# Kernel optimization log

Measured on AMD Instinct MI355X. Metric: run time of the kernel, lower is better.

The kernel has to match this reference:

```python
import jax, jax.numpy as jnp
import numpy as np

SEQ_LEN = 2048
NUM_FILTERS = 24
INPUT_DIM = 256
OUTPUT_DIM = 256
BATCH = 2
N_FFT = 4096  # nearest power of two >= 2*SEQ_LEN - 1


def _spectral_filters(L, k):
    # Hankel matrix Z_{ij} = 2 / ((i+j)^3 - (i+j)), top-k eigvecs scaled by sigma^{1/4}
    e = np.arange(1, L + 1, dtype=np.float64)
    ipj = e[:, None] + e[None, :]
    Z = 2.0 / (ipj ** 3 - ipj)
    sigma, vecs = np.linalg.eigh(Z)
    phi = vecs[:, -k:] * (sigma[-k:] ** 0.25)
    return jnp.asarray(phi, dtype=jnp.float32)


def setup_inputs() -> dict:
    key = jax.random.key(0)
    k1, k2, k3 = jax.random.split(key, 3)
    scale = (NUM_FILTERS * INPUT_DIM) ** (-0.5)
    return {
        "x": jax.random.normal(k1, (BATCH, SEQ_LEN, INPUT_DIM), jnp.float32),
        "phi": _spectral_filters(SEQ_LEN, NUM_FILTERS),  # [L, K]
        "M_phi_plus": jax.random.normal(k2, (NUM_FILTERS, INPUT_DIM, OUTPUT_DIM), jnp.float32) * scale,
        "M_phi_minus": jax.random.normal(k3, (NUM_FILTERS, INPUT_DIM, OUTPUT_DIM), jnp.float32) * scale,
    }


def _convolve(x, phi, n):
    # Faithful port of flash-stu convolve() with use_approx=False.
    B, L, I = x.shape
    K = phi.shape[1]
    # alternating sign (+1, -1, +1, ...) along the sequence
    sgn = jnp.where(jnp.arange(L) % 2 == 0, 1.0, -1.0).astype(x.dtype)[None, :, None, None]  # (1,L,1,1)
    v = jnp.fft.rfft(phi, n=n, axis=0)[None, :, :, None, None]  # (1, n//2+1, K, 1, 1)
    u = jnp.broadcast_to(x[:, :, None, :, None], (B, L, K, I, 1))  # (B,L,K,I,1)
    U = jnp.concatenate([u, u * sgn[..., None]], axis=-1)          # (B,L,K,I,2)
    U_f = jnp.fft.rfft(U, n=n, axis=1)                             # (B,n//2+1,K,I,2)
    U_conv = jnp.fft.irfft(v * U_f, n=n, axis=1)[:, :L]            # (B,L,K,I,2)
    U_plus = U_conv[..., 0]
    U_minus = U_conv[..., 1] * sgn                                 # (B,L,K,I)
    return U_plus, U_minus


def reference(x, phi, M_phi_plus, M_phi_minus):
    U_plus, U_minus = _convolve(x, phi, N_FFT)
    spectral_plus = jnp.einsum('blki,kio->blo', U_plus, M_phi_plus)
    spectral_minus = jnp.einsum('blki,kio->blo', U_minus, M_phi_minus)
    return spectral_plus + spectral_minus
```

## Files before the change

kernel.cpp:

```cpp
#include <hip/hip_runtime.h>
#include <hip/hip_bf16.h>

#define SL 2048
#define NK 24
#define NI 256
#define NO 256
#define NB 2
#define NC 48
#define TD 64

typedef __bf16 bf16x8 __attribute__((ext_vector_type(8)));
typedef float f32x4 __attribute__((ext_vector_type(4)));
typedef unsigned short u16x8 __attribute__((ext_vector_type(8)));
typedef unsigned short ushort_t;
typedef unsigned int u32;

#define OFF_T   0ull
#define SZ_T    (35ull*48*64*64*2)
#define OFF_MT  (OFF_T + SZ_T)
#define SZ_MT   (48ull*256*256*2)
#define OFF_XB  (OFF_MT + SZ_MT)
#define SZ_XB   (2ull*2048*256*2)
#define OFF_YT  (OFF_XB + SZ_XB)
#define SZ_YT   (2ull*48*256*2048*2)
#define WS_NEED (OFF_YT + SZ_YT)

__device__ __forceinline__ unsigned short f2bf(float f) {
    unsigned int u = __float_as_uint(f);
    unsigned int r = (u + 0x7FFFu + ((u >> 16) & 1u)) >> 16;
    return (unsigned short)r;
}

__device__ __forceinline__ void glds16(ushort_t* l, const ushort_t* g) {
    __builtin_amdgcn_global_load_lds((const __attribute__((address_space(1))) u32*)g,
                                     (__attribute__((address_space(3))) u32*)l, 16, 0, 0);
}

__global__ void k_cvt_x(const float* __restrict__ x, ushort_t* __restrict__ xb) {
    int i = blockIdx.x * blockDim.x + threadIdx.x;
    float4 v = reinterpret_cast<const float4*>(x)[i];
    ushort4 o;
    o.x = f2bf(v.x); o.y = f2bf(v.y); o.z = f2bf(v.z); o.w = f2bf(v.w);
    reinterpret_cast<ushort4*>(xb)[i] = o;
}

__global__ void k_mt(const float* __restrict__ Mp, const float* __restrict__ Mm,
                     ushort_t* __restrict__ mt) {
    __shared__ float tile[64][65];
    int c = blockIdx.x, it = blockIdx.y, ot = blockIdx.z;
    int k = c >> 1;
    const float* M = (c & 1) ? Mm : Mp;
    int tid = threadIdx.x;
    int col = tid & 63, rq = tid >> 6;
    for (int rr = 0; rr < 64; rr += 4) {
        int i = rr + rq;
        tile[i][col] = M[((k * NI) + (it * 64 + i)) * NO + ot * 64 + col];
    }
    __syncthreads();
    for (int rr = 0; rr < 64; rr += 4) {
        int o = rr + rq;
        mt[((c * NO) + (ot * 64 + o)) * NI + it * 64 + col] = f2bf(tile[col][o]);
    }
}

__global__ void k_toep(const float* __restrict__ phi, ushort_t* __restrict__ T) {
    int d = (int)blockIdx.x - 3, c = blockIdx.y;
    int ti = threadIdx.x;
    int k = c >> 1, odd = c & 1;
    for (int li = 0; li < TD; ++li) {
        int s = d * TD + li - ti;
        float v = 0.f;
        if (s >= 0 && s < SL) {
            v = phi[s * NK + k];
            if (odd && (s & 1)) v = -v;
        }
        T[(((blockIdx.x) * NC + c) * TD + li) * TD + ti] = f2bf(v);
    }
}

__global__ __launch_bounds__(256, 3) void k_gemm1(const ushort_t* __restrict__ XB,
                                                  const ushort_t* __restrict__ MT,
                                                  ushort_t* __restrict__ yt) {
    __shared__ ushort_t sh[17408];
    int nb_ = blockIdx.x;
    int rb  = blockIdx.y;
    int n0 = nb_ * 128;
    int tid = threadIdx.x, lane = tid & 63, wid = tid >> 6;
    int wr = wid >> 1, wc = wid & 1;
    int ln15 = lane & 15, lq = lane >> 4;
    int swz = lq ^ ((ln15 >> 1) & 3);

    const ushort_t* Arow = XB + (size_t)(rb * 128) * 256;
    const ushort_t* Brow = MT + (size_t)n0 * 256;

    auto stage = [&](int bufsel, int s) {
        ushort_t* L = sh + bufsel * 8192;
        int k0 = s * 32;
#pragma unroll
        for (int jj = 0; jj < 2; ++jj) {
            int flat = tid + jj * 256;
            int row = flat >> 2;
            int k8s = (flat & 3) ^ ((flat >> 3) & 3);
            glds16(L + flat * 8, Arow + row * 256 + k0 + k8s * 8);
        }
#pragma unroll
        for (int jj = 0; jj < 2; ++jj) {
            int flat = tid + jj * 256;
            int row = flat >> 2;
            int k8s = (flat & 3) ^ ((flat >> 3) & 3);
            glds16(L + 4096 + flat * 8, Brow + row * 256 + k0 + k8s * 8);
        }
    };

    f32x4 acc[4][4];
    f32x4 z = {0.f, 0.f, 0.f, 0.f};
#pragma unroll
    for (int mi = 0; mi < 4; ++mi)
#pragma unroll
        for (int ni = 0; ni < 4; ++ni) acc[mi][ni] = z;

    stage(0, 0);
    __syncthreads();
    for (int s = 0; s < 8; ++s) {
        int cur = s & 1;
        if (s < 7) stage(cur ^ 1, s + 1);
        const ushort_t* Ab = sh + cur * 8192;
        const ushort_t* Bb = Ab + 4096;
        bf16x8 af[4], bfr[4];
#pragma unroll
        for (int mi = 0; mi < 4; ++mi)
            af[mi] = *reinterpret_cast<const bf16x8*>(Ab + (wr * 64 + mi * 16 + ln15) * 32 + swz * 8);
#pragma unroll
        for (int ni = 0; ni < 4; ++ni)
            bfr[ni] = *reinterpret_cast<const bf16x8*>(Bb + (wc * 64 + ni * 16 + ln15) * 32 + swz * 8);
#pragma unroll
        for (int mi = 0; mi < 4; ++mi)
#pragma unroll
            for (int ni = 0; ni < 4; ++ni)
                acc[mi][ni] = __builtin_amdgcn_mfma_f32_16x16x32_bf16(af[mi], bfr[ni], acc[mi][ni], 0, 0, 0);
        __syncthreads();
    }

    ushort_t* OT = sh;
#pragma unroll
    for (int mi = 0; mi < 4; ++mi)
#pragma unroll
        for (int ni = 0; ni < 4; ++ni) {
            int t_loc = wr * 64 + mi * 16 + lq * 4;
            int n_loc = wc * 64 + ni * 16 + ln15;
            ushort4 pk;
            pk.x = f2bf(acc[mi][ni][0]);
            pk.y = f2bf(acc[mi][ni][1]);
            pk.z = f2bf(acc[mi][ni][2]);
            pk.w = f2bf(acc[mi][ni][3]);
            *reinterpret_cast<ushort4*>(OT + n_loc * 136 + t_loc) = pk;
        }
    __syncthreads();
    int b = rb >> 4, t0 = (rb & 15) * 128;
#pragma unroll
    for (int jj = 0; jj < 8; ++jj) {
        int flat = tid + jj * 256;
        int n_loc = flat >> 4, te = (flat & 15) * 8;
        int nn = n0 + n_loc;
        int c = nn >> 8, o = nn & 255;
        *reinterpret_cast<u16x8*>(yt + ((size_t)(b * NC + c) * NO + o) * SL + t0 + te) =
            *reinterpret_cast<const u16x8*>(OT + n_loc * 136 + te);
    }
}

#define LOAD_SET(SA, SB, SLOT, AB, BB) do {                                        \
    _Pragma("unroll") for (int m = 0; m < 8; ++m)                                  \
        SA[m] = *(const bf16x8*)((AB) + aBase + (SLOT) + m * 2048);                \
    _Pragma("unroll") for (int n2 = 0; n2 < 4; ++n2)                               \
        SB[n2] = *(const bf16x8*)((BB) + bBase + (SLOT) + n2 * 2048);              \
} while (0)

#define MFMA_SET(SA, SB) do {                                                      \
    _Pragma("unroll") for (int m = 0; m < 8; ++m)                                  \
    _Pragma("unroll") for (int n2 = 0; n2 < 4; ++n2)                               \
        acc[m][n2] = __builtin_amdgcn_mfma_f32_16x16x32_bf16(                      \
            SA[m], SB[n2], acc[m][n2], 0, 0, 0);                                   \
} while (0)

__global__ __launch_bounds__(512, 2) void k_conv8(const ushort_t* __restrict__ Tb,
                                                  const ushort_t* __restrict__ yt,
                                                  float* __restrict__ out) {
    __shared__ ushort_t sh[65536];

    int blk = blockIdx.x;
    int orig = (blk & 7) * 32 + (blk >> 3);
    const int NBt[8] = {4, 7, 11, 14, 18, 21, 25, 28};
    int b_ = orig >> 7;
    int j = orig & 127;
    int pp = 0, base = 0;
    while (pp < 7 && j >= base + NBt[pp]) { base += NBt[pp]; ++pp; }
    int idx = j - base, n = NBt[pp];
    int U = 192 * (pp + 1);
    int u0 = idx * U / n, u1 = (idx + 1) * U / n;

    int tid = threadIdx.x, lane = tid & 63, wid = tid >> 6;
    int wr = wid >> 2, wc = wid & 3;
    int ln15 = lane & 15, lq = lane >> 4;

    const ushort_t* YTb = yt + ((size_t)(b_ * NC * NO) << 11);
    const char* shc = (const char*)sh;

    int s0l = (lq ^ (ln15 & 7)) * 16;
    int s1l = ((4 + lq) ^ (ln15 & 7)) * 16;
    int aBase = (wr * 128 + ln15) * 128;
    int bBase = (wc * 64 + ln15) * 128;
    int gAl = (tid >> 3) * 64 + ((tid & 7) ^ ((tid >> 3) & 7)) * 8;
    int gBl = ((tid >> 3) & 31) * 2048 + ((tid & 7) ^ ((tid >> 3) & 7)) * 8;
    int w2  = wid >> 2;
    int dAl = tid * 8;
    int dBl = w2 * 4096 + (wid & 3) * 512 + lane * 8;

    auto stageA = [&](ushort_t* L, int tt, int c) {
#pragma unroll
        for (int jj = 0; jj < 2; ++jj)
#pragma unroll
            for (int qm = 0; qm < 2; ++qm) {
                int slot = 4 * pp + jj * 2 + qm - tt + 3;
                glds16(L + jj * 8192 + qm * 4096 + dAl,
                       Tb + (((size_t)(slot * NC + c)) << 12) + gAl);
            }
    };
    auto stageB = [&](ushort_t* L, int tt, int c) {
#pragma unroll
        for (int jj = 0; jj < 2; ++jj)
#pragma unroll
            for (int qn = 0; qn < 2; ++qn) {
                int rowS = (jj * 2 + w2) * 64 + qn * 32;
                glds16(L + jj * 8192 + qn * 2048 + dBl,
                       YTb + (((size_t)(c * NO + rowS)) << 11) + tt * 64 + gBl);
            }
    };
    auto stageU = [&](int u) {
        int tt = u / 48, c = u - tt * 48;
        stageA(sh + ((u & 1) << 14), tt, c);
        stageB(sh + 32768 + ((u & 1) << 14), tt, c);
    };

    f32x4 acc[8][4];
    f32x4 z = {0.f, 0.f, 0.f, 0.f};
#pragma unroll
    for (int mi = 0; mi < 8; ++mi)
#pragma unroll
        for (int ni = 0; ni < 4; ++ni) acc[mi][ni] = z;

    bf16x8 s0a[8], s0b[4], s1a[8], s1b[4];

    stageU(u0);
    stageU(u0 + 1);
    asm volatile("s_waitcnt vmcnt(8)" ::: "memory");
    asm volatile("s_barrier" ::: "memory");
    {
        const char* AB = shc + ((u0 & 1) << 15);
        const char* BB = shc + 65536 + ((u0 & 1) << 15);
        LOAD_SET(s0a, s0b, s0l, AB, BB);
    }

    for (int s = u0; s < u1; ++s) {
        const char* AB = shc + ((s & 1) << 15);
        const char* BB = shc + 65536 + ((s & 1) << 15);

        LOAD_SET(s1a, s1b, s1l, AB, BB);
        __builtin_amdgcn_sched_barrier(0);

        __builtin_amdgcn_s_setprio(1);
        MFMA_SET(s0a, s0b);
        __builtin_amdgcn_s_setprio(0);

        asm volatile("s_waitcnt lgkmcnt(0)" ::: "memory");
        asm volatile("s_waitcnt vmcnt(0)" ::: "memory");
        __builtin_amdgcn_sched_barrier(0);
        asm volatile("s_barrier" ::: "memory");

        if (s + 2 < u1) stageU(s + 2);

        if (s + 1 < u1) {
            const char* AB2 = shc + (((s + 1) & 1) << 15);
            const char* BB2 = shc + 65536 + (((s + 1) & 1) << 15);
            LOAD_SET(s0a, s0b, s0l, AB2, BB2);
        }
        __builtin_amdgcn_sched_barrier(0);

        __builtin_amdgcn_s_setprio(1);
        MFMA_SET(s1a, s1b);
        __builtin_amdgcn_s_setprio(0);
        __builtin_amdgcn_sched_barrier(0);
    }

    float* outp = out + (((size_t)b_ * SL) + (size_t)pp * 256) * NO;
#pragma unroll
    for (int mi = 0; mi < 8; ++mi)
#pragma unroll
        for (int ni = 0; ni < 4; ++ni) {
            int l = wr * 128 + mi * 16 + lq * 4;
            int o = wc * 64 + ni * 16 + ln15;
#pragma unroll
            for (int r = 0; r < 4; ++r)
                atomicAdd(&outp[(size_t)(l + r) * NO + o], acc[mi][ni][r]);
        }
}

extern "C" void kernel_launch(void* const* d_in, const int* in_sizes, int n_in,
                              void* d_out, int out_size, void* d_ws, size_t ws_size,
                              hipStream_t stream) {
    const float* x   = (const float*)d_in[0];
    const float* phi = (const float*)d_in[1];
    const float* Mp  = (const float*)d_in[2];
    const float* Mm  = (const float*)d_in[3];
    float* out = (float*)d_out;

    if (ws_size < WS_NEED) return;

    char* ws = (char*)d_ws;
    ushort_t* T  = (ushort_t*)(ws + OFF_T);
    ushort_t* MT = (ushort_t*)(ws + OFF_MT);
    ushort_t* XB = (ushort_t*)(ws + OFF_XB);
    ushort_t* YT = (ushort_t*)(ws + OFF_YT);

    hipMemsetAsync(d_out, 0, (size_t)out_size * sizeof(float), stream);
    k_cvt_x<<<dim3(262144 / 256), dim3(256), 0, stream>>>(x, XB);
    k_mt<<<dim3(48, 4, 4), dim3(256), 0, stream>>>(Mp, Mm, MT);
    k_toep<<<dim3(35, 48), dim3(64), 0, stream>>>(phi, T);
    k_gemm1<<<dim3(96, 32), dim3(256), 0, stream>>>(XB, MT, YT);
    k_conv8<<<dim3(256), dim3(512), 0, stream>>>(T, YT, out);
}
```

Before: 222.0 us.

## Load A operand fragments directly from global memory, keep only B in LDS

```diff
diff --git a/kernel.cpp b/kernel.cpp
--- a/kernel.cpp
+++ b/kernel.cpp
@@ -168,11 +168,14 @@
     }
 }
 
-#define LOAD_SET(SA, SB, SLOT, AB, BB) do {                                        \
+#define LOAD_B_DS(DST, SLOT, BB) do {                                              \
+    _Pragma("unroll") for (int n2 = 0; n2 < 4; ++n2)                               \
+        DST[n2] = *(const bf16x8*)((BB) + bBase + (SLOT) + n2 * 2048);             \
+} while (0)
+
+#define LOAD_A_G(DST, BASE, KHOFF) do {                                            \
     _Pragma("unroll") for (int m = 0; m < 8; ++m)                                  \
-        SA[m] = *(const bf16x8*)((AB) + aBase + (SLOT) + m * 2048);                \
-    _Pragma("unroll") for (int n2 = 0; n2 < 4; ++n2)                               \
-        SB[n2] = *(const bf16x8*)((BB) + bBase + (SLOT) + n2 * 2048);              \
+        DST[m] = *(const bf16x8*)((BASE) + (m >> 2) * 196608 + (m & 3) * 1024 + (KHOFF)); \
 } while (0)
 
 #define MFMA_SET(SA, SB) do {                                                      \
@@ -185,7 +188,7 @@
 __global__ __launch_bounds__(512, 2) void k_conv8(const ushort_t* __restrict__ Tb,
                                                   const ushort_t* __restrict__ yt,
                                                   float* __restrict__ out) {
-    __shared__ ushort_t sh[65536];
+    __shared__ ushort_t sh[32768];
 
     int blk = blockIdx.x;
     int orig = (blk & 7) * 32 + (blk >> 3);
@@ -207,24 +210,15 @@
 
     int s0l = (lq ^ (ln15 & 7)) * 16;
     int s1l = ((4 + lq) ^ (ln15 & 7)) * 16;
-    int aBase = (wr * 128 + ln15) * 128;
     int bBase = (wc * 64 + ln15) * 128;
-    int gAl = (tid >> 3) * 64 + ((tid & 7) ^ ((tid >> 3) & 7)) * 8;
     int gBl = ((tid >> 3) & 31) * 2048 + ((tid & 7) ^ ((tid >> 3) & 7)) * 8;
     int w2  = wid >> 2;
-    int dAl = tid * 8;
     int dBl = w2 * 4096 + (wid & 3) * 512 + lane * 8;
-
-    auto stageA = [&](ushort_t* L, int tt, int c) {
-#pragma unroll
-        for (int jj = 0; jj < 2; ++jj)
-#pragma unroll
-            for (int qm = 0; qm < 2; ++qm) {
-                int slot = 4 * pp + jj * 2 + qm - tt + 3;
-                glds16(L + jj * 8192 + qm * 4096 + dAl,
-                       Tb + (((size_t)(slot * NC + c)) << 12) + gAl);
-            }
+    const ushort_t* aWbase = Tb + wr * 393216 + ln15 * 64 + lq * 8;
+    auto aTile = [&](int tt, int c) {
+        return aWbase + (size_t)((4 * pp + 3 - tt) * 48 + c) * 4096;
     };
+
     auto stageB = [&](ushort_t* L, int tt, int c) {
 #pragma unroll
         for (int jj = 0; jj < 2; ++jj)
@@ -235,11 +229,6 @@
                        YTb + (((size_t)(c * NO + rowS)) << 11) + tt * 64 + gBl);
             }
     };
-    auto stageU = [&](int u) {
-        int tt = u / 48, c = u - tt * 48;
-        stageA(sh + ((u & 1) << 14), tt, c);
-        stageB(sh + 32768 + ((u & 1) << 14), tt, c);
-    };
 
     f32x4 acc[8][4];
     f32x4 z = {0.f, 0.f, 0.f, 0.f};
@@ -248,47 +237,56 @@
 #pragma unroll
         for (int ni = 0; ni < 4; ++ni) acc[mi][ni] = z;
 
-    bf16x8 s0a[8], s0b[4], s1a[8], s1b[4];
-
-    stageU(u0);
-    stageU(u0 + 1);
-    asm volatile("s_waitcnt vmcnt(8)" ::: "memory");
+    int tc = u0 / 48, cc = u0 - tc * 48;
+    int t1 = tc, c1 = cc;
+    if (++c1 == 48) { c1 = 0; ++t1; }
+    int t2 = t1, c2 = c1;
+    if (++c2 == 48) { c2 = 0; ++t2; }
+
+    bf16x8 aC[8], bC[4];
+
+    stageB(sh + ((u0 & 1) << 14), tc, cc);
+    stageB(sh + (((u0 + 1) & 1) << 14), t1, c1);
+    asm volatile("s_waitcnt vmcnt(4)" ::: "memory");
     asm volatile("s_barrier" ::: "memory");
     {
-        const char* AB = shc + ((u0 & 1) << 15);
-        const char* BB = shc + 65536 + ((u0 & 1) << 15);
-        LOAD_SET(s0a, s0b, s0l, AB, BB);
+        const char* BB0 = shc + ((u0 & 1) << 15);
+        LOAD_B_DS(bC, s0l, BB0);
+        LOAD_A_G(aC, aTile(tc, cc), 0);
     }
 
     for (int s = u0; s < u1; ++s) {
-        const char* AB = shc + ((s & 1) << 15);
-        const char* BB = shc + 65536 + ((s & 1) << 15);
-
-        LOAD_SET(s1a, s1b, s1l, AB, BB);
+        const char* BBc = shc + ((s & 1) << 15);
+        const char* BBn = shc + (((s + 1) & 1) << 15);
+        bf16x8 aN[8], bN[4];
+
+        LOAD_B_DS(bN, s1l, BBc);
+        LOAD_A_G(aN, aTile(tc, cc), 32);
         __builtin_amdgcn_sched_barrier(0);
 
         __builtin_amdgcn_s_setprio(1);
-        MFMA_SET(s0a, s0b);
+        MFMA_SET(aC, bC);
         __builtin_amdgcn_s_setprio(0);
 
         asm volatile("s_waitcnt lgkmcnt(0)" ::: "memory");
-        asm volatile("s_waitcnt vmcnt(0)" ::: "memory");
+        asm volatile("s_waitcnt vmcnt(16)" ::: "memory");
         __builtin_amdgcn_sched_barrier(0);
         asm volatile("s_barrier" ::: "memory");
-
-        if (s + 2 < u1) stageU(s + 2);
-
+        __builtin_amdgcn_sched_barrier(0);
+
+        if (s + 2 < u1) stageB(sh + ((s & 1) << 14), t2, c2);
         if (s + 1 < u1) {
-            const char* AB2 = shc + (((s + 1) & 1) << 15);
-            const char* BB2 = shc + 65536 + (((s + 1) & 1) << 15);
-            LOAD_SET(s0a, s0b, s0l, AB2, BB2);
+            LOAD_B_DS(bC, s0l, BBn);
+            LOAD_A_G(aC, aTile(t1, c1), 0);
         }
         __builtin_amdgcn_sched_barrier(0);
 
         __builtin_amdgcn_s_setprio(1);
-        MFMA_SET(s1a, s1b);
+        MFMA_SET(aN, bN);
         __builtin_amdgcn_s_setprio(0);
-        __builtin_amdgcn_sched_barrier(0);
+
+        tc = t1; cc = c1; t1 = t2; c1 = c2;
+        if (++c2 == 48) { c2 = 0; ++t2; }
     }
 
     float* outp = out + (((size_t)b_ * SL) + (size_t)pp * 256) * NO;
```

Result: slower. 349.5 us (+57.4%).
